# Performance work log

Hardware: AMD Instinct MI355X
Metric: run time of the kernel (lower is better)

The kernel has to match this reference:

```python
import jax, jax.numpy as jnp
import numpy as np

N_NODES = 100_000
N_EDGES = 1_600_000
F_IN = 64
HID = 128
HEAD_H = 256
OUT = 32
N_GRAPHS = 512
NEG_SLOPE = 0.01  # torch.nn.LeakyReLU default


def _leaky(v):
    return jnp.where(v >= 0, v, NEG_SLOPE * v)


def _gine_layer(x, src, dst, edge_attr, We, be, Wn, bn, n_nodes):
    # GINEConv (eps=0): nn( x_i + sum_j relu(x_j + lin(edge_attr_ji)) )
    msg = jax.nn.relu(x[src] + edge_attr @ We + be)          # [E, in]
    agg = jax.ops.segment_sum(msg, dst, num_segments=n_nodes)  # [N, in]
    return (agg + x) @ Wn + bn                                # [N, hid]


def setup_inputs() -> dict:
    key = jax.random.key(0)
    ks = jax.random.split(key, 24)
    inp = {}
    inp["x"] = jax.random.normal(ks[0], (N_NODES, F_IN), dtype=jnp.float32)
    inp["edge_index"] = jax.random.randint(ks[1], (2, N_EDGES), 0, N_NODES, dtype=jnp.int32)
    inp["edge_attr"] = jax.random.normal(ks[2], (N_EDGES, 2), dtype=jnp.float32)
    inp["batch"] = jnp.sort(jax.random.randint(ks[3], (N_NODES,), 0, N_GRAPHS, dtype=jnp.int32))
    # GINE layers: edge lin (2 -> in) and nn Linear (in -> hid)
    dims = [F_IN, HID, HID]
    ki = 4
    for l, d_in in enumerate(dims):
        inp[f"We{l}"] = jax.random.normal(ks[ki], (2, d_in), dtype=jnp.float32) / np.sqrt(2.0); ki += 1
        inp[f"be{l}"] = jnp.zeros((d_in,), dtype=jnp.float32)
        inp[f"Wn{l}"] = jax.random.normal(ks[ki], (d_in, HID), dtype=jnp.float32) / np.sqrt(d_in); ki += 1
        inp[f"bn{l}"] = jnp.zeros((HID,), dtype=jnp.float32)
    # head MLP
    inp["Wh0"] = jax.random.normal(ks[ki], (HID, HEAD_H), dtype=jnp.float32) / np.sqrt(HID); ki += 1
    inp["bh0"] = jnp.zeros((HEAD_H,), dtype=jnp.float32)
    inp["Wh1"] = jax.random.normal(ks[ki], (HEAD_H, OUT), dtype=jnp.float32) / np.sqrt(HEAD_H); ki += 1
    inp["bh1"] = jnp.zeros((OUT,), dtype=jnp.float32)
    return inp


def reference(x, edge_index, edge_attr, batch,
              We0, be0, Wn0, bn0,
              We1, be1, Wn1, bn1,
              We2, be2, Wn2, bn2,
              Wh0, bh0, Wh1, bh1):
    src, dst = edge_index[0], edge_index[1]
    h = _leaky(_gine_layer(x, src, dst, edge_attr, We0, be0, Wn0, bn0, N_NODES))
    h = _leaky(_gine_layer(h, src, dst, edge_attr, We1, be1, Wn1, bn1, N_NODES))
    h = _leaky(_gine_layer(h, src, dst, edge_attr, We2, be2, Wn2, bn2, N_NODES))
    pooled = jax.ops.segment_sum(h, batch, num_segments=N_GRAPHS)  # [G, HID]
    h = _leaky(pooled @ Wh0 + bh0)
    return h @ Wh1 + bh1  # [G, OUT]
```

## Files before the change

kernel.cpp:

```cpp
#include <hip/hip_runtime.h>
#include <hip/hip_bf16.h>

#define N_NODES 100000
#define N_EDGES 1600000
#define F_IN 64
#define HID 128
#define HEAD_H 256
#define OUT_F 32
#define N_GRAPHS 512
#define NBK 98
#define BCHUNK 4096
#define NCHUNKS ((N_EDGES + BCHUNK - 1) / BCHUNK)

typedef float f2v __attribute__((ext_vector_type(2)));
typedef short bf16x8 __attribute__((ext_vector_type(8)));
typedef float f32x4 __attribute__((ext_vector_type(4)));

__device__ __forceinline__ float leaky(float v) {
    return v >= 0.f ? v : 0.01f * v;
}

__device__ __forceinline__ float bf2f(ushort u) {
    union { uint i; float f; } c; c.i = ((uint)u) << 16; return c.f;
}

__device__ __forceinline__ ushort f2bf(float f) {
    union { float f; uint i; } c; c.f = f;
    uint r = c.i + 0x7FFF + ((c.i >> 16) & 1);
    return (ushort)(r >> 16);
}

__global__ __launch_bounds__(256) void cast_kernel(const float* __restrict__ x,
                                                   ushort* __restrict__ xb, int n2) {
    int i = blockIdx.x * 256 + threadIdx.x;
    if (i < n2) {
        float2 v = ((const float2*)x)[i];
        uint u = (uint)f2bf(v.x) | ((uint)f2bf(v.y) << 16);
        ((uint*)xb)[i] = u;
    }
}

__global__ __launch_bounds__(256) void prep_wnT(const float* __restrict__ Wn0,
                                                const float* __restrict__ Wn1,
                                                const float* __restrict__ Wn2,
                                                ushort* __restrict__ w0T,
                                                ushort* __restrict__ w1T,
                                                ushort* __restrict__ w2T) {
    int id = blockIdx.x * 256 + threadIdx.x;
    if (id < 128 * 64) {
        int j = id / 64, k = id % 64;
        w0T[id] = f2bf(Wn0[k * 128 + j]);
    } else if (id < 128 * 64 + 128 * 128) {
        int t = id - 128 * 64; int j = t / 128, k = t % 128;
        w1T[t] = f2bf(Wn1[k * 128 + j]);
    } else if (id < 128 * 64 + 2 * 128 * 128) {
        int t = id - 128 * 64 - 128 * 128; int j = t / 128, k = t % 128;
        w2T[t] = f2bf(Wn2[k * 128 + j]);
    }
}


__global__ __launch_bounds__(256) void bucket_hist(const int* __restrict__ dst,
                                                   int* __restrict__ cnt98) {
    __shared__ int h[NBK];
    int tid = threadIdx.x;
    if (tid < NBK) h[tid] = 0;
    __syncthreads();
    int e0 = blockIdx.x * BCHUNK;
    int nn = N_EDGES - e0; if (nn > BCHUNK) nn = BCHUNK;
    for (int i = tid; i < nn; i += 256) {
        atomicAdd(&h[dst[e0 + i] >> 10], 1);
    }
    __syncthreads();
    if (tid < NBK && h[tid] > 0) atomicAdd(&cnt98[tid], h[tid]);
}

__global__ __launch_bounds__(128) void bucket_scan(const int* __restrict__ cnt98,
                                                   int* __restrict__ bbase,
                                                   int* __restrict__ bcur,
                                                   int* __restrict__ rowptr) {
    __shared__ int sd[128];
    int t = threadIdx.x;
    int v = (t < NBK) ? cnt98[t] : 0;
    sd[t] = v;
    __syncthreads();
    for (int off = 1; off < 128; off <<= 1) {
        int u = (t >= off) ? sd[t - off] : 0;
        __syncthreads();
        sd[t] += u;
        __syncthreads();
    }
    if (t < NBK) {
        int ex = sd[t] - v;
        bbase[t] = ex;
        bcur[t] = ex;
    }
    if (t == 0) {
        bbase[NBK] = N_EDGES;
        rowptr[N_NODES] = N_EDGES;
    }
}

__global__ __launch_bounds__(256) void bin_kernel(const int* __restrict__ src,
                                                  const int* __restrict__ dst,
                                                  const float2* __restrict__ ea,
                                                  int* __restrict__ bcur,
                                                  uint2* __restrict__ recs1) {
    __shared__ int hist[NBK], tmp[NBK], offs[NBK], cur[NBK], gbase[NBK];
    __shared__ uint2 stage[BCHUNK];
    __shared__ unsigned char sbid[BCHUNK];

    int tid = threadIdx.x;
    int e0 = blockIdx.x * BCHUNK;
    int nn = N_EDGES - e0; if (nn > BCHUNK) nn = BCHUNK;

    if (tid < NBK) hist[tid] = 0;
    __syncthreads();

    for (int i = tid; i < nn; i += 256) {
        atomicAdd(&hist[dst[e0 + i] >> 10], 1);
    }
    __syncthreads();

    if (tid < NBK) tmp[tid] = hist[tid];
    __syncthreads();
    for (int off = 1; off < NBK; off <<= 1) {
        int u = (tid < NBK && tid >= off) ? tmp[tid - off] : 0;
        __syncthreads();
        if (tid < NBK) tmp[tid] += u;
        __syncthreads();
    }
    if (tid < NBK) {
        int ex = tmp[tid] - hist[tid];
        offs[tid] = ex;
        cur[tid] = ex;
        gbase[tid] = (hist[tid] > 0) ? atomicAdd(&bcur[tid], hist[tid]) : 0;
    }
    __syncthreads();

    for (int i = tid; i < nn; i += 256) {
        int e = e0 + i;
        int d = dst[e];
        int b = d >> 10;
        int dloc = d & 1023;
        float2 a = ea[e];
        uint2 r;
        r.x = (uint)src[e] | ((uint)dloc << 22);
        r.y = (uint)f2bf(a.x) | ((uint)f2bf(a.y) << 16);
        int pos = atomicAdd(&cur[b], 1);
        stage[pos] = r;
        sbid[pos] = (unsigned char)b;
    }
    __syncthreads();

    for (int i = tid; i < nn; i += 256) {
        int b = sbid[i];
        recs1[gbase[b] + (i - offs[b])] = stage[i];
    }
}

__global__ __launch_bounds__(256) void order_kernel(const uint2* __restrict__ recs1,
                                                    const int* __restrict__ bbase,
                                                    int* __restrict__ rowptr,
                                                    uint2* __restrict__ recs2) {
    __shared__ int h[1024];
    __shared__ int ssum[256];
    int b = blockIdx.x;
    int tid = threadIdx.x;
    int base = bbase[b];
    int end = bbase[b + 1];

    for (int i = tid; i < 1024; i += 256) h[i] = 0;
    __syncthreads();

    for (int t = base + tid; t < end; t += 256) {
        atomicAdd(&h[recs1[t].x >> 22], 1);
    }
    __syncthreads();

    int i4 = tid * 4;
    int a0 = h[i4], a1 = h[i4 + 1], a2 = h[i4 + 2], a3 = h[i4 + 3];
    int s = a0 + a1 + a2 + a3;
    ssum[tid] = s;
    __syncthreads();
    for (int off = 1; off < 256; off <<= 1) {
        int u = (tid >= off) ? ssum[tid - off] : 0;
        __syncthreads();
        ssum[tid] += u;
        __syncthreads();
    }
    int pre = base + ssum[tid] - s;
    int c0 = pre, c1 = pre + a0, c2 = c1 + a1, c3 = c2 + a2;
    h[i4] = c0; h[i4 + 1] = c1; h[i4 + 2] = c2; h[i4 + 3] = c3;

    int n = (b << 10) + i4;
    if (n + 4 <= N_NODES) {
        *(int4*)(rowptr + n) = make_int4(c0, c1, c2, c3);
    } else {
        if (n + 0 < N_NODES) rowptr[n + 0] = c0;
        if (n + 1 < N_NODES) rowptr[n + 1] = c1;
        if (n + 2 < N_NODES) rowptr[n + 2] = c2;
        if (n + 3 < N_NODES) rowptr[n + 3] = c3;
    }
    __syncthreads();

    for (int t = base + tid; t < end; t += 256) {
        uint2 r = recs1[t];
        int pos = atomicAdd(&h[r.x >> 22], 1);
        recs2[pos] = make_uint2(r.x & 0x3FFFFFu, r.y);
    }
}


template <int K>
__global__ __launch_bounds__(256) void gine_fused(const ushort* __restrict__ xb,
                                                  const uint2* __restrict__ recs,
                                                  const int* __restrict__ rowptr,
                                                  const float* __restrict__ We,
                                                  const float* __restrict__ be,
                                                  const ushort* __restrict__ wnT,
                                                  const float* __restrict__ bn,
                                                  ushort* __restrict__ hb) {
    __shared__ float tile[16 * K];
    int tid = threadIdx.x;
    int wave = tid >> 6;
    int lane = tid & 63;
    int n0 = blockIdx.x * 16;

    if constexpr (K == 128) {
        int j = lane * 2;
        f2v w0v = {We[j], We[j + 1]};
        f2v w1v = {We[128 + j], We[128 + j + 1]};
        f2v bbv = {be[j], be[j + 1]};
        const f2v zero = {0.f, 0.f};

        for (int q = 0; q < 4; q++) {
            int node = n0 + wave * 4 + q;
            int rs = __builtin_amdgcn_readfirstlane(rowptr[node]);
            int re = __builtin_amdgcn_readfirstlane(rowptr[node + 1]);
            f2v accv = {0.f, 0.f};

            auto proc = [&](uint2 r, uint u) {
                float ax = bf2f((ushort)(r.y & 0xFFFF));
                float ay = bf2f((ushort)(r.y >> 16));
                union { uint i; float f; } lo, hi;
                lo.i = u << 16;
                hi.i = u & 0xFFFF0000u;
                f2v xv = {lo.f, hi.f};
                f2v m = xv + bbv;
                m = ay * w1v + m;
                m = ax * w0v + m;
                m = __builtin_elementwise_max(m, zero);
                accv += m;
            };

            int t = rs;
            for (; t + 7 < re; t += 8) {
                uint2 r0 = recs[t];
                uint2 r1 = recs[t + 1];
                uint2 r2 = recs[t + 2];
                uint2 r3 = recs[t + 3];
                uint2 r4 = recs[t + 4];
                uint2 r5 = recs[t + 5];
                uint2 r6 = recs[t + 6];
                uint2 r7 = recs[t + 7];
                uint u0 = *(const uint*)(xb + (size_t)r0.x * 128 + j);
                uint u1 = *(const uint*)(xb + (size_t)r1.x * 128 + j);
                uint u2 = *(const uint*)(xb + (size_t)r2.x * 128 + j);
                uint u3 = *(const uint*)(xb + (size_t)r3.x * 128 + j);
                uint u4 = *(const uint*)(xb + (size_t)r4.x * 128 + j);
                uint u5 = *(const uint*)(xb + (size_t)r5.x * 128 + j);
                uint u6 = *(const uint*)(xb + (size_t)r6.x * 128 + j);
                uint u7 = *(const uint*)(xb + (size_t)r7.x * 128 + j);
                proc(r0, u0); proc(r1, u1); proc(r2, u2); proc(r3, u3);
                proc(r4, u4); proc(r5, u5); proc(r6, u6); proc(r7, u7);
            }
            for (; t + 3 < re; t += 4) {
                uint2 r0 = recs[t];
                uint2 r1 = recs[t + 1];
                uint2 r2 = recs[t + 2];
                uint2 r3 = recs[t + 3];
                uint u0 = *(const uint*)(xb + (size_t)r0.x * 128 + j);
                uint u1 = *(const uint*)(xb + (size_t)r1.x * 128 + j);
                uint u2 = *(const uint*)(xb + (size_t)r2.x * 128 + j);
                uint u3 = *(const uint*)(xb + (size_t)r3.x * 128 + j);
                proc(r0, u0); proc(r1, u1); proc(r2, u2); proc(r3, u3);
            }
            for (; t < re; t++) {
                uint2 r0 = recs[t];
                uint u0 = *(const uint*)(xb + (size_t)r0.x * 128 + j);
                proc(r0, u0);
            }

            int row = node & 15;
            int idx = (row * 128 + j) ^ ((row & 7) << 2);
            *(f2v*)&tile[idx] = accv;
        }
    } else {
        float w0 = We[lane], w1 = We[64 + lane], bb = be[lane];

        for (int q = 0; q < 4; q++) {
            int node = n0 + wave * 4 + q;
            int rs = __builtin_amdgcn_readfirstlane(rowptr[node]);
            int re = __builtin_amdgcn_readfirstlane(rowptr[node + 1]);
            float acc = 0.f;

            auto proc = [&](uint2 r, ushort u) {
                float ax = bf2f((ushort)(r.y & 0xFFFF));
                float ay = bf2f((ushort)(r.y >> 16));
                float m = bf2f(u) + bb;
                m = ay * w1 + m;
                m = ax * w0 + m;
                acc += fmaxf(m, 0.f);
            };

            int t = rs;
            for (; t + 7 < re; t += 8) {
                uint2 r0 = recs[t];
                uint2 r1 = recs[t + 1];
                uint2 r2 = recs[t + 2];
                uint2 r3 = recs[t + 3];
                uint2 r4 = recs[t + 4];
                uint2 r5 = recs[t + 5];
                uint2 r6 = recs[t + 6];
                uint2 r7 = recs[t + 7];
                ushort u0 = xb[(size_t)r0.x * 64 + lane];
                ushort u1 = xb[(size_t)r1.x * 64 + lane];
                ushort u2 = xb[(size_t)r2.x * 64 + lane];
                ushort u3 = xb[(size_t)r3.x * 64 + lane];
                ushort u4 = xb[(size_t)r4.x * 64 + lane];
                ushort u5 = xb[(size_t)r5.x * 64 + lane];
                ushort u6 = xb[(size_t)r6.x * 64 + lane];
                ushort u7 = xb[(size_t)r7.x * 64 + lane];
                proc(r0, u0); proc(r1, u1); proc(r2, u2); proc(r3, u3);
                proc(r4, u4); proc(r5, u5); proc(r6, u6); proc(r7, u7);
            }
            for (; t + 3 < re; t += 4) {
                uint2 r0 = recs[t];
                uint2 r1 = recs[t + 1];
                uint2 r2 = recs[t + 2];
                uint2 r3 = recs[t + 3];
                ushort u0 = xb[(size_t)r0.x * 64 + lane];
                ushort u1 = xb[(size_t)r1.x * 64 + lane];
                ushort u2 = xb[(size_t)r2.x * 64 + lane];
                ushort u3 = xb[(size_t)r3.x * 64 + lane];
                proc(r0, u0); proc(r1, u1); proc(r2, u2); proc(r3, u3);
            }
            for (; t < re; t++) {
                uint2 r0 = recs[t];
                ushort u0 = xb[(size_t)r0.x * 64 + lane];
                proc(r0, u0);
            }

            int row = node & 15;
            int idx = (row * 64 + lane) ^ ((row & 7) << 2);
            tile[idx] = acc;
        }
    }
    __syncthreads();

    {
        int l15 = lane & 15;
        int kgrp = (lane >> 4) * 8;
        int row = l15;
        int sw = (row & 7) << 2;
        int nt0 = wave * 2;
        int nt1 = nt0 + 1;
        float b0 = bn[nt0 * 16 + l15];
        float b1 = bn[nt1 * 16 + l15];
        f32x4 acc0 = {b0, b0, b0, b0};
        f32x4 acc1 = {b1, b1, b1, b1};

#pragma unroll
        for (int kk = 0; kk < K / 32; kk++) {
            int k0 = kk * 32 + kgrp;
            f32x4 p0 = *(const f32x4*)&tile[(row * K + k0) ^ sw];
            f32x4 p1 = *(const f32x4*)&tile[(row * K + k0 + 4) ^ sw];
            bf16x8 xr = *(const bf16x8*)(xb + (size_t)(n0 + row) * K + k0);
            bf16x8 a;
#pragma unroll
            for (int e = 0; e < 4; e++) {
                a[e]     = (short)f2bf(p0[e] + bf2f((ushort)xr[e]));
                a[e + 4] = (short)f2bf(p1[e] + bf2f((ushort)xr[e + 4]));
            }
            bf16x8 bf0 = *(const bf16x8*)(wnT + (size_t)(nt0 * 16 + l15) * K + k0);
            bf16x8 bf1 = *(const bf16x8*)(wnT + (size_t)(nt1 * 16 + l15) * K + k0);
            acc0 = __builtin_amdgcn_mfma_f32_16x16x32_bf16(a, bf0, acc0, 0, 0, 0);
            acc1 = __builtin_amdgcn_mfma_f32_16x16x32_bf16(a, bf1, acc1, 0, 0, 0);
        }

        int rbase = n0 + (lane >> 4) * 4;
#pragma unroll
        for (int r = 0; r < 4; r++) {
            hb[(size_t)(rbase + r) * HID + nt0 * 16 + l15] = f2bf(leaky(acc0[r]));
            hb[(size_t)(rbase + r) * HID + nt1 * 16 + l15] = f2bf(leaky(acc1[r]));
        }
    }
}

#define POOL_NPW 64
__global__ __launch_bounds__(256) void pool_kernel(const ushort* __restrict__ h,
                                                   const int* __restrict__ batch,
                                                   float* __restrict__ pooled) {
    int wid = (blockIdx.x * 256 + (int)threadIdx.x) >> 6;
    int lane = threadIdx.x & 63;
    int n0 = wid * POOL_NPW;
    if (n0 >= N_NODES) return;
    int n1 = n0 + POOL_NPW; if (n1 > N_NODES) n1 = N_NODES;

    int j = lane * 2;
    f2v acc = {0.f, 0.f};
    int g = __builtin_amdgcn_readfirstlane(batch[n0]);
    for (int i = n0; i < n1; i++) {
        int bg = __builtin_amdgcn_readfirstlane(batch[i]);
        if (bg != g) {
            atomicAdd(&pooled[g * HID + j], acc.x);
            atomicAdd(&pooled[g * HID + j + 1], acc.y);
            acc.x = 0.f; acc.y = 0.f;
            g = bg;
        }
        uint u = *(const uint*)(h + (size_t)i * HID + j);
        union { uint i; float f; } lo, hi;
        lo.i = u << 16;
        hi.i = u & 0xFFFF0000u;
        acc.x += lo.f;
        acc.y += hi.f;
    }
    atomicAdd(&pooled[g * HID + j], acc.x);
    atomicAdd(&pooled[g * HID + j + 1], acc.y);
}


__global__ __launch_bounds__(256) void head_kernel(const float* __restrict__ pooled,
                                                   const float* __restrict__ Wh0,
                                                   const float* __restrict__ bh0,
                                                   const float* __restrict__ Wh1,
                                                   const float* __restrict__ bh1,
                                                   float* __restrict__ out) {
    __shared__ float p[HID];
    __shared__ float hid[HEAD_H];
    int g = blockIdx.x;
    int t = threadIdx.x;
    if (t < HID) p[t] = pooled[g * HID + t];
    __syncthreads();
    float acc = bh0[t];
    for (int k = 0; k < HID; k++) acc += p[k] * Wh0[k * HEAD_H + t];
    hid[t] = leaky(acc);
    __syncthreads();
    if (t < OUT_F) {
        float o = bh1[t];
        for (int k = 0; k < HEAD_H; k++) o += hid[k] * Wh1[k * OUT_F + t];
        out[g * OUT_F + t] = o;
    }
}

extern "C" void kernel_launch(void* const* d_in, const int* in_sizes, int n_in,
                              void* d_out, int out_size, void* d_ws, size_t ws_size,
                              hipStream_t stream) {
    const float* x     = (const float*)d_in[0];
    const int*   ei    = (const int*)d_in[1];
    const float* ea    = (const float*)d_in[2];
    const int*   batch = (const int*)d_in[3];
    const float* We0 = (const float*)d_in[4];
    const float* be0 = (const float*)d_in[5];
    const float* Wn0 = (const float*)d_in[6];
    const float* bn0 = (const float*)d_in[7];
    const float* We1 = (const float*)d_in[8];
    const float* be1 = (const float*)d_in[9];
    const float* Wn1 = (const float*)d_in[10];
    const float* bn1 = (const float*)d_in[11];
    const float* We2 = (const float*)d_in[12];
    const float* be2 = (const float*)d_in[13];
    const float* Wn2 = (const float*)d_in[14];
    const float* bn2 = (const float*)d_in[15];
    const float* Wh0 = (const float*)d_in[16];
    const float* bh0 = (const float*)d_in[17];
    const float* Wh1 = (const float*)d_in[18];
    const float* bh1 = (const float*)d_in[19];

    const int* src = ei;
    const int* dst = ei + N_EDGES;

    char* ws = (char*)d_ws;
    size_t o = 0;
    uint2*  recs1 = (uint2*)(ws + o); o += (size_t)N_EDGES * 8;
    uint2*  recs2 = (uint2*)(ws + o); o += (size_t)N_EDGES * 8;
    ushort* xb0  = (ushort*)(ws + o); o += (size_t)N_NODES * 64 * 2;
    ushort* hbufA = (ushort*)(ws + o); o += (size_t)N_NODES * 128 * 2;
    ushort* hbufB = (ushort*)(ws + o); o += (size_t)N_NODES * 128 * 2;
    int*    rowptr = (int*)(ws + o);  o += 400128;
    int*    cnt98  = (int*)(ws + o);  o += 4096;
    int*    bbase  = (int*)(ws + o);  o += 4096;
    int*    bcur   = (int*)(ws + o);  o += 4096;
    ushort* wnT0 = (ushort*)(ws + o); o += 128 * 64 * 2;
    ushort* wnT1 = (ushort*)(ws + o); o += 128 * 128 * 2;
    ushort* wnT2 = (ushort*)(ws + o); o += 128 * 128 * 2;
    float*  pooled = (float*)(ws + o); o += (size_t)N_GRAPHS * HID * 4;

    cast_kernel<<<(N_NODES * F_IN / 2 + 255) / 256, 256, 0, stream>>>(x, xb0, N_NODES * F_IN / 2);
    prep_wnT<<<160, 256, 0, stream>>>(Wn0, Wn1, Wn2, wnT0, wnT1, wnT2);

    hipMemsetAsync(cnt98, 0, NBK * sizeof(int), stream);
    bucket_hist<<<NCHUNKS, 256, 0, stream>>>(dst, cnt98);
    bucket_scan<<<1, 128, 0, stream>>>(cnt98, bbase, bcur, rowptr);
    bin_kernel<<<NCHUNKS, 256, 0, stream>>>(src, dst, (const float2*)ea, bcur, recs1);
    order_kernel<<<NBK, 256, 0, stream>>>(recs1, bbase, rowptr, recs2);

    const int FUSED_BLOCKS = N_NODES / 16;

    gine_fused<64><<<FUSED_BLOCKS, 256, 0, stream>>>(xb0, recs2, rowptr, We0, be0, wnT0, bn0, hbufA);
    gine_fused<128><<<FUSED_BLOCKS, 256, 0, stream>>>(hbufA, recs2, rowptr, We1, be1, wnT1, bn1, hbufB);
    gine_fused<128><<<FUSED_BLOCKS, 256, 0, stream>>>(hbufB, recs2, rowptr, We2, be2, wnT2, bn2, hbufA);

    hipMemsetAsync(pooled, 0, (size_t)N_GRAPHS * HID * sizeof(float), stream);
    pool_kernel<<<(N_NODES / POOL_NPW + 3) / 4, 256, 0, stream>>>(hbufA, batch, pooled);
    head_kernel<<<N_GRAPHS, 256, 0, stream>>>(pooled, Wh0, bh0, Wh1, bh1, (float*)d_out);
}
```

Measured before the change: 367.5 us.

## Give each wave its own 16-node tile to drop block-wide barrier in GINE

Each wave now aggregates all 16 nodes of its own tile and runs the full 16x128 MFMA projection itself, so the block-wide __syncthreads is removed and waves proceed independently. The tile is stored in LDS as bf16 with the self term x folded in before storing, which removes the separate global reload of x rows in the GEMM phase and halves LDS footprint per row. In exchange each wave reloads all eight Wn column tiles instead of two, and per-wave load imbalance across 16 nodes can lengthen tails.

```diff
diff --git a/kernel.cpp b/kernel.cpp
--- a/kernel.cpp
+++ b/kernel.cpp
@@ -11,6 +11,7 @@
 #define NBK 98
 #define BCHUNK 4096
 #define NCHUNKS ((N_EDGES + BCHUNK - 1) / BCHUNK)
+#define N_TASKS (N_NODES / 16)
 
 typedef float f2v __attribute__((ext_vector_type(2)));
 typedef short bf16x8 __attribute__((ext_vector_type(8)));
@@ -221,11 +222,14 @@
                                                   const ushort* __restrict__ wnT,
                                                   const float* __restrict__ bn,
                                                   ushort* __restrict__ hb) {
-    __shared__ float tile[16 * K];
+    __shared__ ushort tile4[4][16 * K];
     int tid = threadIdx.x;
     int wave = tid >> 6;
     int lane = tid & 63;
-    int n0 = blockIdx.x * 16;
+    int wt = blockIdx.x * 4 + wave;
+    if (wt >= N_TASKS) return;
+    char* tile = (char*)tile4[wave];
+    int n0 = wt * 16;
 
     if constexpr (K == 128) {
         int j = lane * 2;
@@ -234,8 +238,8 @@
         f2v bbv = {be[j], be[j + 1]};
         const f2v zero = {0.f, 0.f};
 
-        for (int q = 0; q < 4; q++) {
-            int node = n0 + wave * 4 + q;
+        for (int q = 0; q < 16; q++) {
+            int node = n0 + q;
             int rs = __builtin_amdgcn_readfirstlane(rowptr[node]);
             int re = __builtin_amdgcn_readfirstlane(rowptr[node + 1]);
             f2v accv = {0.f, 0.f};
@@ -292,15 +296,22 @@
                 proc(r0, u0);
             }
 
-            int row = node & 15;
-            int idx = (row * 128 + j) ^ ((row & 7) << 2);
-            *(f2v*)&tile[idx] = accv;
+            {
+                uint u = *(const uint*)(xb + (size_t)node * 128 + j);
+                union { uint i; float f; } lo, hi;
+                lo.i = u << 16;
+                hi.i = u & 0xFFFF0000u;
+                accv.x += lo.f;
+                accv.y += hi.f;
+            }
+            uint up = (uint)f2bf(accv.x) | ((uint)f2bf(accv.y) << 16);
+            *(uint*)(tile + ((q * 256 + lane * 4) ^ ((q & 7) << 4))) = up;
         }
     } else {
         float w0 = We[lane], w1 = We[64 + lane], bb = be[lane];
 
-        for (int q = 0; q < 4; q++) {
-            int node = n0 + wave * 4 + q;
+        for (int q = 0; q < 16; q++) {
+            int node = n0 + q;
             int rs = __builtin_amdgcn_readfirstlane(rowptr[node]);
             int re = __builtin_amdgcn_readfirstlane(rowptr[node + 1]);
             float acc = 0.f;
@@ -352,48 +363,32 @@
                 proc(r0, u0);
             }
 
-            int row = node & 15;
-            int idx = (row * 64 + lane) ^ ((row & 7) << 2);
-            tile[idx] = acc;
+            acc += bf2f(xb[(size_t)node * 64 + lane]);
+            *(ushort*)(tile + ((q * 128 + lane * 2) ^ ((q & 7) << 4))) = f2bf(acc);
         }
     }
-    __syncthreads();
 
     {
         int l15 = lane & 15;
         int kgrp = (lane >> 4) * 8;
-        int row = l15;
-        int sw = (row & 7) << 2;
-        int nt0 = wave * 2;
-        int nt1 = nt0 + 1;
-        float b0 = bn[nt0 * 16 + l15];
-        float b1 = bn[nt1 * 16 + l15];
-        f32x4 acc0 = {b0, b0, b0, b0};
-        f32x4 acc1 = {b1, b1, b1, b1};
+        int sw = (l15 & 7) << 4;
+        int rbase = n0 + (lane >> 4) * 4;
 
 #pragma unroll
-        for (int kk = 0; kk < K / 32; kk++) {
-            int k0 = kk * 32 + kgrp;
-            f32x4 p0 = *(const f32x4*)&tile[(row * K + k0) ^ sw];
-            f32x4 p1 = *(const f32x4*)&tile[(row * K + k0 + 4) ^ sw];
-            bf16x8 xr = *(const bf16x8*)(xb + (size_t)(n0 + row) * K + k0);
-            bf16x8 a;
+        for (int nt = 0; nt < 8; nt++) {
+            float b = bn[nt * 16 + l15];
+            f32x4 acc = {b, b, b, b};
 #pragma unroll
-            for (int e = 0; e < 4; e++) {
-                a[e]     = (short)f2bf(p0[e] + bf2f((ushort)xr[e]));
-                a[e + 4] = (short)f2bf(p1[e] + bf2f((ushort)xr[e + 4]));
-            }
-            bf16x8 bf0 = *(const bf16x8*)(wnT + (size_t)(nt0 * 16 + l15) * K + k0);
-            bf16x8 bf1 = *(const bf16x8*)(wnT + (size_t)(nt1 * 16 + l15) * K + k0);
-            acc0 = __builtin_amdgcn_mfma_f32_16x16x32_bf16(a, bf0, acc0, 0, 0, 0);
-            acc1 = __builtin_amdgcn_mfma_f32_16x16x32_bf16(a, bf1, acc1, 0, 0, 0);
-        }
-
-        int rbase = n0 + (lane >> 4) * 4;
+            for (int kk = 0; kk < K / 32; kk++) {
+                int k0 = kk * 32 + kgrp;
+                bf16x8 a = *(const bf16x8*)(tile + ((l15 * K * 2 + k0 * 2) ^ sw));
+                bf16x8 bf = *(const bf16x8*)(wnT + (size_t)(nt * 16 + l15) * K + k0);
+                acc = __builtin_amdgcn_mfma_f32_16x16x32_bf16(a, bf, acc, 0, 0, 0);
+            }
 #pragma unroll
-        for (int r = 0; r < 4; r++) {
-            hb[(size_t)(rbase + r) * HID + nt0 * 16 + l15] = f2bf(leaky(acc0[r]));
-            hb[(size_t)(rbase + r) * HID + nt1 * 16 + l15] = f2bf(leaky(acc1[r]));
+            for (int r = 0; r < 4; r++) {
+                hb[(size_t)(rbase + r) * HID + nt * 16 + l15] = f2bf(leaky(acc[r]));
+            }
         }
     }
 }
@@ -506,7 +501,7 @@
     bin_kernel<<<NCHUNKS, 256, 0, stream>>>(src, dst, (const float2*)ea, bcur, recs1);
     order_kernel<<<NBK, 256, 0, stream>>>(recs1, bbase, rowptr, recs2);
 
-    const int FUSED_BLOCKS = N_NODES / 16;
+    const int FUSED_BLOCKS = (N_TASKS + 3) / 4;
 
     gine_fused<64><<<FUSED_BLOCKS, 256, 0, stream>>>(xb0, recs2, rowptr, We0, be0, wnT0, bn0, hbufA);
     gine_fused<128><<<FUSED_BLOCKS, 256, 0, stream>>>(hbufA, recs2, rowptr, We1, be1, wnT1, bn1, hbufB);
```

After: 448.6 us. 1.22x slower.
